# Performance work log

Measured on AMD Instinct MI355X. Metric: run time of the kernel, lower is better.

## Reference

```python
import jax, jax.numpy as jnp
import numpy as np

T, D = 4096, 2048      # tokens, hidden
E, I, K = 16, 1408, 4  # experts, moe intermediate, top_k


def setup_inputs() -> dict:
    key = jax.random.key(0)
    ks = jax.random.split(key, 6)
    W_SCALE = 0.05  # keep activations in a sane range
    x = jax.random.normal(ks[0], (T, D), dtype=jnp.float32)
    w0 = jax.random.normal(ks[1], (E, I, D), dtype=jnp.float32) * W_SCALE  # gate proj
    w1 = jax.random.normal(ks[2], (E, I, D), dtype=jnp.float32) * W_SCALE  # up proj
    w2 = jax.random.normal(ks[3], (E, D, I), dtype=jnp.float32) * W_SCALE  # down proj
    selected_experts = jax.random.randint(ks[4], (T, K), 0, E, dtype=jnp.int32)
    rw = jax.random.uniform(ks[5], (T, K), dtype=jnp.float32)
    routing_weights = rw / jnp.sum(rw, axis=-1, keepdims=True)  # normalized top-k weights
    return {"x": x, "w0": w0, "w1": w1, "w2": w2,
            "selected_experts": selected_experts, "routing_weights": routing_weights}


def reference(x, w0, w1, w2, selected_experts, routing_weights):
    # Per-expert SwiGLU FFN over all tokens: y_e = (silu(x W0_e^T) * (x W1_e^T)) W2_e^T
    def expert_fn(w0_e, w1_e, w2_e):
        h = jax.nn.silu(x @ w0_e.T) * (x @ w1_e.T)  # [T, I]
        return h @ w2_e.T                            # [T, D]

    ys = jax.vmap(expert_fn)(w0, w1, w2)             # [E, T, D]
    # Gather each token's top-k expert outputs and apply routing weights.
    tok = jnp.arange(x.shape[0])[:, None]            # [T, 1]
    gathered = ys[selected_experts, tok, :]          # [T, K, D]
    return gathered * routing_weights[:, :, None]    # [T, K, D]
```

## Files before the change

kernel.cpp:

```cpp
#include <hip/hip_runtime.h>
#include <hip/hip_bf16.h>
#include <stdint.h>

#define NT 4096
#define ND 2048
#define NE 16
#define NI 1408
#define NK 4
#define NTK (NT*NK)

typedef __attribute__((ext_vector_type(8))) short bf16x8;
typedef __attribute__((ext_vector_type(4))) float f32x4;

__device__ __forceinline__ short f2b(float f){
  uint32_t u = __float_as_uint(f);
  uint32_t r = (u + 0x7fffu + ((u >> 16) & 1u)) >> 16;
  return (short)(uint16_t)r;
}
__device__ __forceinline__ float b2f(short s){
  return __uint_as_float(((uint32_t)(uint16_t)s) << 16);
}

__device__ __forceinline__ void gl16(const void* g, void* l){
  __builtin_amdgcn_global_load_lds(
      (const __attribute__((address_space(1))) void*)g,
      (__attribute__((address_space(3))) void*)l, 16, 0, 0);
}

__device__ __forceinline__ int xcd_swz(int lin, int nwg){
  int cpx = nwg >> 3;
  return (lin & 7) * cpx + (lin >> 3);
}



__global__ void detect_init_kernel(const unsigned short* xu, int* wsi){
  const int tid = threadIdx.x;
  if (tid < 64) wsi[tid] = 0;
  wsi[3584 + tid] = 0;
  __shared__ int red[256];
  int c = 0;
  for (int i = tid; i < 8192; i += 256){
    int ex = (xu[i] >> 7) & 0xff;
    c += (ex >= 132) ? 1 : 0;
  }
  red[tid] = c;
  __syncthreads();
  if (tid == 0){
    int s = 0;
    for (int i = 0; i < 256; i++) s += red[i];
    wsi[32] = (s < 64) ? 1 : 0;
  }
}

__global__ void hist_kernel(const int* __restrict__ sel, int* wsi){
  int i = blockIdx.x * 256 + threadIdx.x;
  if (i < NTK) atomicAdd(&wsi[sel[i]], 1);
}

__global__ void plan_kernel(int* wsi){
  if (threadIdx.x != 0) return;
  int4* work64  = (int4*)(wsi + 64);
  int4* work128 = (int4*)(wsi + 2048);
  int off = 0, nw = 0, nw128 = 0;
  for (int e = 0; e < NE; e++){
    int c = wsi[e];
    wsi[40 + e] = off;
    for (int mt = 0; mt * 64 < c; mt++){
      int rem = c - mt * 64;
      work64[nw].x = e; work64[nw].y = off + mt * 64;
      work64[nw].z = rem < 64 ? rem : 64; work64[nw].w = 0;
      nw++;
    }
    for (int mt = 0; mt * 128 < c; mt++){
      int rem = c - mt * 128;
      work128[nw128].x = e; work128[nw128].y = off + mt * 128;
      work128[nw128].z = rem < 128 ? rem : 128; work128[nw128].w = 0;
      nw128++;
    }
    off += c;
  }
  wsi[33] = nw;
  wsi[34] = nw128;
}

__global__ void scatter_kernel(const int* __restrict__ sel, int* wsi, int* list){
  int i = blockIdx.x * 256 + threadIdx.x;
  if (i < NTK){
    int e = sel[i];
    int pos = atomicAdd(&wsi[16 + e], 1);
    list[wsi[40 + e] + pos] = i;
  }
}


__global__ __launch_bounds__(256)
void conv_kernel(const float* __restrict__ src, short* __restrict__ dst,
                 int n8, const int* __restrict__ wsi){
  if (wsi[32]) return;
  int stride = gridDim.x * 256;
  for (int i = blockIdx.x * 256 + threadIdx.x; i < n8; i += stride){
    const float4* s = (const float4*)(src + (size_t)i * 8);
    float4 a = s[0], b = s[1];
    bf16x8 v;
    v[0]=f2b(a.x); v[1]=f2b(a.y); v[2]=f2b(a.z); v[3]=f2b(a.w);
    v[4]=f2b(b.x); v[5]=f2b(b.y); v[6]=f2b(b.z); v[7]=f2b(b.w);
    *(bf16x8*)(dst + (size_t)i * 8) = v;
  }
}


template<int ISB>
__global__ __launch_bounds__(256, 2)
void pass1b_kernel(const void* __restrict__ xg, const void* __restrict__ w0g,
                   const void* __restrict__ w1g,
                   const short* __restrict__ xb, const short* __restrict__ w0b,
                   const short* __restrict__ w1b,
                   const int* __restrict__ wsi, const int* __restrict__ list,
                   short* __restrict__ H)
{
  if (wsi[32] != ISB) return;
  const int nmt = wsi[34];
  const int lin = blockIdx.x + 160 * blockIdx.y;
  const int swz = xcd_swz(lin, 160 * gridDim.y);
  const int mtile = swz % 160;
  const int ntile = swz / 160;
  if (mtile >= nmt) return;
  const int4 wk = ((const int4*)(wsi + 2048))[mtile];
  const int e = wk.x, row_base = wk.y, rows = wk.z;
  const int n0 = ntile * 128;

  __shared__ short As [128 * 32];
  __shared__ short B0s[128 * 32];
  __shared__ short B1s[128 * 32];

  const int tid = threadIdx.x;
  const short* xs  = ISB ? (const short*)xg  : xb;
  const short* w0s = ISB ? (const short*)w0g : w0b;
  const short* w1s = ISB ? (const short*)w1g : w1b;
  const short* zp  = (const short*)(wsi + 3584);

  const int rr = tid >> 2;
  const int cc = (tid & 3) << 3;
  const bool va0 = rr < rows;
  const bool va1 = (64 + rr) < rows;
  const int t0 = va0 ? (list[row_base + rr] >> 2) : 0;
  const int t1 = va1 ? (list[row_base + 64 + rr] >> 2) : 0;
  const short* ag0 = va0 ? xs + (size_t)t0 * ND + cc : zp;
  const short* ag1 = va1 ? xs + (size_t)t1 * ND + cc : zp;
  const int sa0 = va0 ? 32 : 0;
  const int sa1 = va1 ? 32 : 0;
  const short* b0g0 = w0s + ((size_t)e * NI + n0 + rr)      * ND + cc;
  const short* b0g1 = w0s + ((size_t)e * NI + n0 + 64 + rr) * ND + cc;
  const short* b1g0 = w1s + ((size_t)e * NI + n0 + rr)      * ND + cc;
  const short* b1g1 = w1s + ((size_t)e * NI + n0 + 64 + rr) * ND + cc;

  short* la0  = &As [(size_t)tid * 8];
  short* la1  = &As [((size_t)tid + 256) * 8];
  short* lb00 = &B0s[(size_t)tid * 8];
  short* lb01 = &B0s[((size_t)tid + 256) * 8];
  short* lb10 = &B1s[(size_t)tid * 8];
  short* lb11 = &B1s[((size_t)tid + 256) * 8];

  const int lane = tid & 63;
  const int wv = tid >> 6;
  const int wm = (wv >> 1) << 6;
  const int wn = (wv & 1) << 6;
  const int r16 = lane & 15;
  const int qd  = lane >> 4;
  const int qd8 = qd << 3;

  f32x4 acc0[4][4] = {};
  f32x4 acc1[4][4] = {};

  for (int kt = 0; kt < ND; kt += 32){
    __syncthreads();
    gl16(ag0,  la0);  gl16(ag1,  la1);
    gl16(b0g0, lb00); gl16(b0g1, lb01);
    gl16(b1g0, lb10); gl16(b1g1, lb11);
    ag0 += sa0; ag1 += sa1;
    b0g0 += 32; b0g1 += 32; b1g0 += 32; b1g1 += 32;
    __syncthreads();
    bf16x8 af[4], b0f[4], b1f[4];
    #pragma unroll
    for (int mi = 0; mi < 4; mi++)
      af[mi] = *(const bf16x8*)&As[(wm + mi*16 + r16) * 32 + qd8];
    #pragma unroll
    for (int ni = 0; ni < 4; ni++){
      b0f[ni] = *(const bf16x8*)&B0s[(wn + ni*16 + r16) * 32 + qd8];
      b1f[ni] = *(const bf16x8*)&B1s[(wn + ni*16 + r16) * 32 + qd8];
    }
    #pragma unroll
    for (int mi = 0; mi < 4; mi++)
      #pragma unroll
      for (int ni = 0; ni < 4; ni++){
        acc0[mi][ni] = __builtin_amdgcn_mfma_f32_16x16x32_bf16(af[mi], b0f[ni], acc0[mi][ni], 0, 0, 0);
        acc1[mi][ni] = __builtin_amdgcn_mfma_f32_16x16x32_bf16(af[mi], b1f[ni], acc1[mi][ni], 0, 0, 0);
      }
  }

  #pragma unroll
  for (int mi = 0; mi < 4; mi++){
    #pragma unroll
    for (int r = 0; r < 4; r++){
      int m = wm + mi*16 + qd*4 + r;
      if (m >= rows) continue;
      size_t hrow = (size_t)(row_base + m) * NI + n0 + wn;
      #pragma unroll
      for (int ni = 0; ni < 4; ni++){
        float a0v = acc0[mi][ni][r];
        float a1v = acc1[mi][ni][r];
        float hv = (a0v / (1.f + __expf(-a0v))) * a1v;
        H[hrow + ni*16 + r16] = f2b(hv);
      }
    }
  }
}


template<int ISB>
__global__ __launch_bounds__(256, 2)
void pass2b_kernel(const void* __restrict__ w2g, const void* __restrict__ rw,
                   const short* __restrict__ w2b,
                   const int* __restrict__ wsi, const int* __restrict__ list,
                   const short* __restrict__ H, void* __restrict__ out)
{
  if (wsi[32] != ISB) return;
  const int nmt = wsi[34];
  const int lin = blockIdx.x + 160 * blockIdx.y;
  const int swz = xcd_swz(lin, 160 * gridDim.y);
  const int mtile = swz % 160;
  const int ntile = swz / 160;
  if (mtile >= nmt) return;
  const int4 wk = ((const int4*)(wsi + 2048))[mtile];
  const int e = wk.x, row_base = wk.y, rows = wk.z;
  const int n0 = ntile * 256;

  __shared__ short As[128 * 32];
  __shared__ short Bs[256 * 32];

  const int tid = threadIdx.x;
  const short* ws2 = ISB ? (const short*)w2g : w2b;
  const short* zp  = (const short*)(wsi + 3584);

  const int rr = tid >> 2;
  const int cc = (tid & 3) << 3;
  const bool va0 = rr < rows;
  const bool va1 = (64 + rr) < rows;
  const short* ag0 = va0 ? H + (size_t)(row_base + rr) * NI + cc : zp;
  const short* ag1 = va1 ? H + (size_t)(row_base + 64 + rr) * NI + cc : zp;
  const int sa0 = va0 ? 32 : 0;
  const int sa1 = va1 ? 32 : 0;
  const short* bg0 = ws2 + ((size_t)e * ND + n0 + rr)       * NI + cc;
  const short* bg1 = ws2 + ((size_t)e * ND + n0 + 64  + rr) * NI + cc;
  const short* bg2 = ws2 + ((size_t)e * ND + n0 + 128 + rr) * NI + cc;
  const short* bg3 = ws2 + ((size_t)e * ND + n0 + 192 + rr) * NI + cc;

  short* la0 = &As[(size_t)tid * 8];
  short* la1 = &As[((size_t)tid + 256) * 8];
  short* lb0 = &Bs[(size_t)tid * 8];
  short* lb1 = &Bs[((size_t)tid + 256) * 8];
  short* lb2 = &Bs[((size_t)tid + 512) * 8];
  short* lb3 = &Bs[((size_t)tid + 768) * 8];

  const int lane = tid & 63;
  const int wv = tid >> 6;
  const int wm = (wv >> 1) << 6;
  const int wn = (wv & 1) << 7;
  const int r16 = lane & 15;
  const int qd  = lane >> 4;
  const int qd8 = qd << 3;

  f32x4 acc[4][8] = {};

  for (int kt = 0; kt < NI; kt += 32){
    __syncthreads();
    gl16(ag0, la0); gl16(ag1, la1);
    gl16(bg0, lb0); gl16(bg1, lb1);
    gl16(bg2, lb2); gl16(bg3, lb3);
    ag0 += sa0; ag1 += sa1;
    bg0 += 32; bg1 += 32; bg2 += 32; bg3 += 32;
    __syncthreads();
    bf16x8 af[4], bf[8];
    #pragma unroll
    for (int mi = 0; mi < 4; mi++)
      af[mi] = *(const bf16x8*)&As[(wm + mi*16 + r16) * 32 + qd8];
    #pragma unroll
    for (int ni = 0; ni < 8; ni++)
      bf[ni] = *(const bf16x8*)&Bs[(wn + ni*16 + r16) * 32 + qd8];
    #pragma unroll
    for (int mi = 0; mi < 4; mi++)
      #pragma unroll
      for (int ni = 0; ni < 8; ni++)
        acc[mi][ni] = __builtin_amdgcn_mfma_f32_16x16x32_bf16(af[mi], bf[ni], acc[mi][ni], 0, 0, 0);
  }

  #pragma unroll
  for (int mi = 0; mi < 4; mi++){
    #pragma unroll
    for (int r = 0; r < 4; r++){
      int m = wm + mi*16 + qd*4 + r;
      if (m >= rows) continue;
      int p = list[row_base + m];
      float sc = ISB ? b2f(((const short*)rw)[p]) : ((const float*)rw)[p];
      size_t orow = (size_t)p * ND + n0 + wn;
      #pragma unroll
      for (int ni = 0; ni < 8; ni++){
        float v = acc[mi][ni][r] * sc;
        if (ISB) ((short*)out)[orow + ni*16 + r16] = f2b(v);
        else     ((float*)out)[orow + ni*16 + r16] = v;
      }
    }
  }
}


template<int ISB>
__device__ __forceinline__ void stage8(short* dst, const void* base, size_t off, bool valid){
  if (ISB){
    bf16x8 v = valid ? *(const bf16x8*)((const short*)base + off) : (bf16x8)0;
    *(bf16x8*)dst = v;
  } else {
    if (valid){
      const float4* s = (const float4*)((const float*)base + off);
      float4 a = s[0], b = s[1];
      dst[0]=f2b(a.x); dst[1]=f2b(a.y); dst[2]=f2b(a.z); dst[3]=f2b(a.w);
      dst[4]=f2b(b.x); dst[5]=f2b(b.y); dst[6]=f2b(b.z); dst[7]=f2b(b.w);
    } else {
      *(bf16x8*)dst = (bf16x8)0;
    }
  }
}

#define LDS_STRIDE 40

template<int ISB>
__global__ __launch_bounds__(256)
void pass1_kernel(const void* __restrict__ x, const void* __restrict__ w0,
                  const void* __restrict__ w1, const int* __restrict__ wsi,
                  const int* __restrict__ list, short* __restrict__ H)
{
  if (wsi[32] != ISB) return;
  if ((int)blockIdx.x >= wsi[33]) return;
  const int4 wk = ((const int4*)(wsi + 64))[blockIdx.x];
  const int e = wk.x, row_base = wk.y, rows = wk.z;
  const int n0 = blockIdx.y * 64;

  __shared__ short As [64 * LDS_STRIDE];
  __shared__ short B0s[64 * LDS_STRIDE];
  __shared__ short B1s[64 * LDS_STRIDE];

  const int tid = threadIdx.x;
  const int lr  = tid >> 2;
  const int c8  = (tid & 3) << 3;
  const bool avalid = lr < rows;
  size_t abase = 0;
  if (avalid){
    int tok = list[row_base + lr] >> 2;
    abase = (size_t)tok * ND + c8;
  }
  const size_t bbase = ((size_t)e * NI + (size_t)(n0 + lr)) * (size_t)ND + c8;

  const int lane = tid & 63;
  const int wv = tid >> 6;
  const int wm = (wv >> 1) << 5;
  const int wn = (wv & 1) << 5;
  const int r16 = lane & 15;
  const int qd  = lane >> 4;
  const int qd8 = qd << 3;

  f32x4 acc0[2][2] = {};
  f32x4 acc1[2][2] = {};

  short* a_dst  = &As [lr * LDS_STRIDE + c8];
  short* b0_dst = &B0s[lr * LDS_STRIDE + c8];
  short* b1_dst = &B1s[lr * LDS_STRIDE + c8];

  for (int kt = 0; kt < ND; kt += 32){
    __syncthreads();
    stage8<ISB>(a_dst,  x,  abase + kt, avalid);
    stage8<ISB>(b0_dst, w0, bbase + kt, true);
    stage8<ISB>(b1_dst, w1, bbase + kt, true);
    __syncthreads();
    bf16x8 af[2], b0f[2], b1f[2];
    #pragma unroll
    for (int mi = 0; mi < 2; mi++)
      af[mi] = *(const bf16x8*)&As[(wm + mi*16 + r16) * LDS_STRIDE + qd8];
    #pragma unroll
    for (int ni = 0; ni < 2; ni++){
      b0f[ni] = *(const bf16x8*)&B0s[(wn + ni*16 + r16) * LDS_STRIDE + qd8];
      b1f[ni] = *(const bf16x8*)&B1s[(wn + ni*16 + r16) * LDS_STRIDE + qd8];
    }
    #pragma unroll
    for (int mi = 0; mi < 2; mi++)
      #pragma unroll
      for (int ni = 0; ni < 2; ni++){
        acc0[mi][ni] = __builtin_amdgcn_mfma_f32_16x16x32_bf16(af[mi], b0f[ni], acc0[mi][ni], 0, 0, 0);
        acc1[mi][ni] = __builtin_amdgcn_mfma_f32_16x16x32_bf16(af[mi], b1f[ni], acc1[mi][ni], 0, 0, 0);
      }
  }

  #pragma unroll
  for (int mi = 0; mi < 2; mi++){
    #pragma unroll
    for (int r = 0; r < 4; r++){
      int m = wm + mi*16 + qd*4 + r;
      if (m >= rows) continue;
      size_t hrow = (size_t)(row_base + m) * NI + n0;
      #pragma unroll
      for (int ni = 0; ni < 2; ni++){
        float a0v = acc0[mi][ni][r];
        float a1v = acc1[mi][ni][r];
        float hv = (a0v / (1.f + __expf(-a0v))) * a1v;
        H[hrow + wn + ni*16 + r16] = f2b(hv);
      }
    }
  }
}

template<int ISB>
__global__ __launch_bounds__(256)
void pass2_kernel(const void* __restrict__ w2, const void* __restrict__ rw,
                  const int* __restrict__ wsi, const int* __restrict__ list,
                  const short* __restrict__ H, void* __restrict__ out)
{
  if (wsi[32] != ISB) return;
  if ((int)blockIdx.x >= wsi[33]) return;
  const int4 wk = ((const int4*)(wsi + 64))[blockIdx.x];
  const int e = wk.x, row_base = wk.y, rows = wk.z;
  const int n0 = blockIdx.y * 64;

  __shared__ short As[64 * LDS_STRIDE];
  __shared__ short Bs[64 * LDS_STRIDE];

  const int tid = threadIdx.x;
  const int lr  = tid >> 2;
  const int c8  = (tid & 3) << 3;
  const bool avalid = lr < rows;
  const size_t abase = (size_t)(row_base + lr) * NI + c8;
  const size_t bbase = ((size_t)e * ND + (size_t)(n0 + lr)) * (size_t)NI + c8;

  const int lane = tid & 63;
  const int wv = tid >> 6;
  const int wm = (wv >> 1) << 5;
  const int wn = (wv & 1) << 5;
  const int r16 = lane & 15;
  const int qd  = lane >> 4;
  const int qd8 = qd << 3;

  f32x4 acc[2][2] = {};

  short* a_dst = &As[lr * LDS_STRIDE + c8];
  short* b_dst = &Bs[lr * LDS_STRIDE + c8];

  for (int kt = 0; kt < NI; kt += 32){
    __syncthreads();
    {
      bf16x8 v = avalid ? *(const bf16x8*)&H[abase + kt] : (bf16x8)0;
      *(bf16x8*)a_dst = v;
    }
    stage8<ISB>(b_dst, w2, bbase + kt, true);
    __syncthreads();
    bf16x8 af[2], bf[2];
    #pragma unroll
    for (int mi = 0; mi < 2; mi++)
      af[mi] = *(const bf16x8*)&As[(wm + mi*16 + r16) * LDS_STRIDE + qd8];
    #pragma unroll
    for (int ni = 0; ni < 2; ni++)
      bf[ni] = *(const bf16x8*)&Bs[(wn + ni*16 + r16) * LDS_STRIDE + qd8];
    #pragma unroll
    for (int mi = 0; mi < 2; mi++)
      #pragma unroll
      for (int ni = 0; ni < 2; ni++)
        acc[mi][ni] = __builtin_amdgcn_mfma_f32_16x16x32_bf16(af[mi], bf[ni], acc[mi][ni], 0, 0, 0);
  }

  #pragma unroll
  for (int mi = 0; mi < 2; mi++){
    #pragma unroll
    for (int r = 0; r < 4; r++){
      int m = wm + mi*16 + qd*4 + r;
      if (m >= rows) continue;
      int p = list[row_base + m];
      float sc = ISB ? b2f(((const short*)rw)[p]) : ((const float*)rw)[p];
      size_t orow = (size_t)p * ND + n0;
      #pragma unroll
      for (int ni = 0; ni < 2; ni++){
        float v = acc[mi][ni][r] * sc;
        if (ISB) ((short*)out)[orow + wn + ni*16 + r16] = f2b(v);
        else     ((float*)out)[orow + wn + ni*16 + r16] = v;
      }
    }
  }
}


extern "C" void kernel_launch(void* const* d_in, const int* in_sizes, int n_in,
                              void* d_out, int out_size, void* d_ws, size_t ws_size,
                              hipStream_t stream) {
  (void)in_sizes; (void)n_in; (void)out_size;
  const void* x  = d_in[0];
  const void* w0 = d_in[1];
  const void* w1 = d_in[2];
  const void* w2 = d_in[3];
  const int* sel = (const int*)d_in[4];
  const void* rw = d_in[5];

  int* wsi   = (int*)d_ws;
  int* list  = wsi + 4096;
  short* H   = (short*)((char*)d_ws + 262144);

  const size_t H_BYTES  = (size_t)NTK * NI * 2;
  const size_t XB_BYTES = (size_t)NT * ND * 2;
  const size_t WB_BYTES = (size_t)NE * NI * ND * 2;
  const size_t offX = 262144 + H_BYTES;
  const size_t offW = offX + XB_BYTES;
  const size_t need = offW + 2 * WB_BYTES;

  detect_init_kernel<<<1, 256, 0, stream>>>((const unsigned short*)x, wsi);
  hist_kernel<<<NTK/256, 256, 0, stream>>>(sel, wsi);
  plan_kernel<<<1, 64, 0, stream>>>(wsi);
  scatter_kernel<<<NTK/256, 256, 0, stream>>>(sel, wsi, list);

  if (ws_size >= need){
    short* xb  = (short*)((char*)d_ws + offX);
    short* w0b = (short*)((char*)d_ws + offW);
    short* w1b = w0b + (size_t)NE * NI * ND;
    short* w2b = w0b;

    conv_kernel<<<2048, 256, 0, stream>>>((const float*)x,  xb,  NT*ND/8,    wsi);
    conv_kernel<<<2048, 256, 0, stream>>>((const float*)w0, w0b, NE*NI*ND/8, wsi);
    conv_kernel<<<2048, 256, 0, stream>>>((const float*)w1, w1b, NE*NI*ND/8, wsi);

    dim3 g1(160, NI/128);
    pass1b_kernel<1><<<g1, 256, 0, stream>>>(x, w0, w1, xb, w0b, w1b, wsi, list, H);
    pass1b_kernel<0><<<g1, 256, 0, stream>>>(x, w0, w1, xb, w0b, w1b, wsi, list, H);

    conv_kernel<<<2048, 256, 0, stream>>>((const float*)w2, w2b, NE*ND*NI/8, wsi);

    dim3 g2(160, ND/256);
    pass2b_kernel<1><<<g2, 256, 0, stream>>>(w2, rw, w2b, wsi, list, H, d_out);
    pass2b_kernel<0><<<g2, 256, 0, stream>>>(w2, rw, w2b, wsi, list, H, d_out);
  } else {
    dim3 g1(272, NI/64);
    dim3 g2(272, ND/64);
    pass1_kernel<1><<<g1, 256, 0, stream>>>(x, w0, w1, wsi, list, H);
    pass1_kernel<0><<<g1, 256, 0, stream>>>(x, w0, w1, wsi, list, H);
    pass2_kernel<1><<<g2, 256, 0, stream>>>(w2, rw, wsi, list, H, d_out);
    pass2_kernel<0><<<g2, 256, 0, stream>>>(w2, rw, wsi, list, H, d_out);
  }
}
```

Before: 1.130 ms.

## Double-buffer LDS in grouped GEMMs, fuse fp32-to-bf16 conversions, parallelize plan

Both grouped GEMM passes now keep two LDS stages, so the global-to-LDS loads for the next K-slice are issued before the MFMAs on the current one, with a single barrier per iteration. This hides load latency that two barriers per step used to expose, at the cost of doubled LDS use, which may limit occupancy. When the workspace is large enough, the four fp32-to-bf16 conversion launches become one fused kernel over x, w0, w1 and w2 into separate buffers. The plan kernel computes its prefix sums with wave shuffles across lanes instead of a serial loop on one thread.

```diff
diff --git a/kernel.cpp b/kernel.cpp
--- a/kernel.cpp
+++ b/kernel.cpp
@@ -59,29 +59,33 @@
 }
 
 __global__ void plan_kernel(int* wsi){
-  if (threadIdx.x != 0) return;
-  int4* work64  = (int4*)(wsi + 64);
-  int4* work128 = (int4*)(wsi + 2048);
-  int off = 0, nw = 0, nw128 = 0;
+  const int lane = threadIdx.x;
+  int c = (lane < NE) ? wsi[lane] : 0;
+  int off = 0, tb128 = 0, tb64 = 0;
+  int nm128 = (c + 127) >> 7;
+  int nm64  = (c + 63) >> 6;
   for (int e = 0; e < NE; e++){
-    int c = wsi[e];
-    wsi[40 + e] = off;
-    for (int mt = 0; mt * 64 < c; mt++){
+    int ce  = __shfl(c, e, 64);
+    int t1  = __shfl(nm128, e, 64);
+    int t0  = __shfl(nm64, e, 64);
+    if (e < lane){ off += ce; tb128 += t1; tb64 += t0; }
+  }
+  if (lane < NE){
+    wsi[40 + lane] = off;
+    int4* work128 = (int4*)(wsi + 2048);
+    for (int mt = 0; mt < nm128; mt++){
+      int rem = c - mt * 128;
+      work128[tb128 + mt] = make_int4(lane, off + mt * 128, rem < 128 ? rem : 128, 0);
+    }
+    int4* work64 = (int4*)(wsi + 64);
+    for (int mt = 0; mt < nm64; mt++){
       int rem = c - mt * 64;
-      work64[nw].x = e; work64[nw].y = off + mt * 64;
-      work64[nw].z = rem < 64 ? rem : 64; work64[nw].w = 0;
-      nw++;
-    }
-    for (int mt = 0; mt * 128 < c; mt++){
-      int rem = c - mt * 128;
-      work128[nw128].x = e; work128[nw128].y = off + mt * 128;
-      work128[nw128].z = rem < 128 ? rem : 128; work128[nw128].w = 0;
-      nw128++;
-    }
-    off += c;
-  }
-  wsi[33] = nw;
-  wsi[34] = nw128;
+      work64[tb64 + mt] = make_int4(lane, off + mt * 64, rem < 64 ? rem : 64, 0);
+    }
+  }
+  int tot128 = __shfl(tb128 + nm128, NE - 1, 64);
+  int tot64  = __shfl(tb64 + nm64, NE - 1, 64);
+  if (lane == 0){ wsi[33] = tot64; wsi[34] = tot128; }
 }
 
 __global__ void scatter_kernel(const int* __restrict__ sel, int* wsi, int* list){
@@ -95,17 +99,37 @@
 
 
 __global__ __launch_bounds__(256)
-void conv_kernel(const float* __restrict__ src, short* __restrict__ dst,
-                 int n8, const int* __restrict__ wsi){
+void conv1_kernel(const float* __restrict__ src, short* __restrict__ dst,
+                  long n4, const int* __restrict__ wsi){
   if (wsi[32]) return;
-  int stride = gridDim.x * 256;
-  for (int i = blockIdx.x * 256 + threadIdx.x; i < n8; i += stride){
-    const float4* s = (const float4*)(src + (size_t)i * 8);
-    float4 a = s[0], b = s[1];
-    bf16x8 v;
-    v[0]=f2b(a.x); v[1]=f2b(a.y); v[2]=f2b(a.z); v[3]=f2b(a.w);
-    v[4]=f2b(b.x); v[5]=f2b(b.y); v[6]=f2b(b.z); v[7]=f2b(b.w);
-    *(bf16x8*)(dst + (size_t)i * 8) = v;
+  const long stride = (long)gridDim.x * 256;
+  for (long i = (long)blockIdx.x * 256 + threadIdx.x; i < n4; i += stride){
+    float4 a = ((const float4*)src)[i];
+    short4 v; v.x = f2b(a.x); v.y = f2b(a.y); v.z = f2b(a.z); v.w = f2b(a.w);
+    *(short4*)(dst + i * 4) = v;
+  }
+}
+
+__global__ __launch_bounds__(256)
+void conv4_kernel(const float* __restrict__ x, const float* __restrict__ w0,
+                  const float* __restrict__ w1, const float* __restrict__ w2,
+                  short* __restrict__ xb, short* __restrict__ w0b,
+                  short* __restrict__ w1b, short* __restrict__ w2b,
+                  const int* __restrict__ wsi){
+  if (wsi[32]) return;
+  const long NX = (long)NT * ND / 4;
+  const long NW = (long)NE * NI * ND / 4;
+  const long total = NX + 3 * NW;
+  const long stride = (long)gridDim.x * 256;
+  for (long i = (long)blockIdx.x * 256 + threadIdx.x; i < total; i += stride){
+    const float4* s; short* d; long j;
+    if (i < NX)            { s = (const float4*)x;  d = xb;  j = i; }
+    else if (i < NX + NW)  { s = (const float4*)w0; d = w0b; j = i - NX; }
+    else if (i < NX + 2*NW){ s = (const float4*)w1; d = w1b; j = i - NX - NW; }
+    else                   { s = (const float4*)w2; d = w2b; j = i - NX - 2*NW; }
+    float4 a = s[j];
+    short4 v; v.x = f2b(a.x); v.y = f2b(a.y); v.z = f2b(a.z); v.w = f2b(a.w);
+    *(short4*)(d + j * 4) = v;
   }
 }
 
@@ -130,9 +154,9 @@
   const int e = wk.x, row_base = wk.y, rows = wk.z;
   const int n0 = ntile * 128;
 
-  __shared__ short As [128 * 32];
-  __shared__ short B0s[128 * 32];
-  __shared__ short B1s[128 * 32];
+  __shared__ short As [2 * 128 * 32];
+  __shared__ short B0s[2 * 128 * 32];
+  __shared__ short B1s[2 * 128 * 32];
 
   const int tid = threadIdx.x;
   const short* xs  = ISB ? (const short*)xg  : xb;
@@ -173,22 +197,32 @@
   f32x4 acc0[4][4] = {};
   f32x4 acc1[4][4] = {};
 
-  for (int kt = 0; kt < ND; kt += 32){
-    __syncthreads();
-    gl16(ag0,  la0);  gl16(ag1,  la1);
-    gl16(b0g0, lb00); gl16(b0g1, lb01);
-    gl16(b1g0, lb10); gl16(b1g1, lb11);
-    ag0 += sa0; ag1 += sa1;
-    b0g0 += 32; b0g1 += 32; b1g0 += 32; b1g1 += 32;
-    __syncthreads();
+  const int nst = ND / 32;
+  gl16(ag0,  la0);  gl16(ag1,  la1);
+  gl16(b0g0, lb00); gl16(b0g1, lb01);
+  gl16(b1g0, lb10); gl16(b1g1, lb11);
+  ag0 += sa0; ag1 += sa1;
+  b0g0 += 32; b0g1 += 32; b1g0 += 32; b1g1 += 32;
+  __syncthreads();
+
+  for (int t = 0; t < nst; ++t){
+    const int bo = (t & 1) << 12;
+    const int bn = ((t + 1) & 1) << 12;
     bf16x8 af[4], b0f[4], b1f[4];
     #pragma unroll
     for (int mi = 0; mi < 4; mi++)
-      af[mi] = *(const bf16x8*)&As[(wm + mi*16 + r16) * 32 + qd8];
+      af[mi] = *(const bf16x8*)&As[bo + (wm + mi*16 + r16) * 32 + qd8];
     #pragma unroll
     for (int ni = 0; ni < 4; ni++){
-      b0f[ni] = *(const bf16x8*)&B0s[(wn + ni*16 + r16) * 32 + qd8];
-      b1f[ni] = *(const bf16x8*)&B1s[(wn + ni*16 + r16) * 32 + qd8];
+      b0f[ni] = *(const bf16x8*)&B0s[bo + (wn + ni*16 + r16) * 32 + qd8];
+      b1f[ni] = *(const bf16x8*)&B1s[bo + (wn + ni*16 + r16) * 32 + qd8];
+    }
+    if (t + 1 < nst){
+      gl16(ag0,  la0  + bn); gl16(ag1,  la1  + bn);
+      gl16(b0g0, lb00 + bn); gl16(b0g1, lb01 + bn);
+      gl16(b1g0, lb10 + bn); gl16(b1g1, lb11 + bn);
+      ag0 += sa0; ag1 += sa1;
+      b0g0 += 32; b0g1 += 32; b1g0 += 32; b1g1 += 32;
     }
     #pragma unroll
     for (int mi = 0; mi < 4; mi++)
@@ -197,6 +231,7 @@
         acc0[mi][ni] = __builtin_amdgcn_mfma_f32_16x16x32_bf16(af[mi], b0f[ni], acc0[mi][ni], 0, 0, 0);
         acc1[mi][ni] = __builtin_amdgcn_mfma_f32_16x16x32_bf16(af[mi], b1f[ni], acc1[mi][ni], 0, 0, 0);
       }
+    __syncthreads();
   }
 
   #pragma unroll
@@ -236,8 +271,8 @@
   const int e = wk.x, row_base = wk.y, rows = wk.z;
   const int n0 = ntile * 256;
 
-  __shared__ short As[128 * 32];
-  __shared__ short Bs[256 * 32];
+  __shared__ short As[2 * 128 * 32];
+  __shared__ short Bs[2 * 256 * 32];
 
   const int tid = threadIdx.x;
   const short* ws2 = ISB ? (const short*)w2g : w2b;
@@ -273,26 +308,39 @@
 
   f32x4 acc[4][8] = {};
 
-  for (int kt = 0; kt < NI; kt += 32){
-    __syncthreads();
-    gl16(ag0, la0); gl16(ag1, la1);
-    gl16(bg0, lb0); gl16(bg1, lb1);
-    gl16(bg2, lb2); gl16(bg3, lb3);
-    ag0 += sa0; ag1 += sa1;
-    bg0 += 32; bg1 += 32; bg2 += 32; bg3 += 32;
-    __syncthreads();
+  const int nst = NI / 32;
+  gl16(ag0, la0); gl16(ag1, la1);
+  gl16(bg0, lb0); gl16(bg1, lb1);
+  gl16(bg2, lb2); gl16(bg3, lb3);
+  ag0 += sa0; ag1 += sa1;
+  bg0 += 32; bg1 += 32; bg2 += 32; bg3 += 32;
+  __syncthreads();
+
+  for (int t = 0; t < nst; ++t){
+    const int abo = (t & 1) << 12;
+    const int abn = ((t + 1) & 1) << 12;
+    const int bbo = (t & 1) << 13;
+    const int bbn = ((t + 1) & 1) << 13;
     bf16x8 af[4], bf[8];
     #pragma unroll
     for (int mi = 0; mi < 4; mi++)
-      af[mi] = *(const bf16x8*)&As[(wm + mi*16 + r16) * 32 + qd8];
+      af[mi] = *(const bf16x8*)&As[abo + (wm + mi*16 + r16) * 32 + qd8];
     #pragma unroll
     for (int ni = 0; ni < 8; ni++)
-      bf[ni] = *(const bf16x8*)&Bs[(wn + ni*16 + r16) * 32 + qd8];
+      bf[ni] = *(const bf16x8*)&Bs[bbo + (wn + ni*16 + r16) * 32 + qd8];
+    if (t + 1 < nst){
+      gl16(ag0, la0 + abn); gl16(ag1, la1 + abn);
+      gl16(bg0, lb0 + bbn); gl16(bg1, lb1 + bbn);
+      gl16(bg2, lb2 + bbn); gl16(bg3, lb3 + bbn);
+      ag0 += sa0; ag1 += sa1;
+      bg0 += 32; bg1 += 32; bg2 += 32; bg3 += 32;
+    }
     #pragma unroll
     for (int mi = 0; mi < 4; mi++)
       #pragma unroll
       for (int ni = 0; ni < 8; ni++)
         acc[mi][ni] = __builtin_amdgcn_mfma_f32_16x16x32_bf16(af[mi], bf[ni], acc[mi][ni], 0, 0, 0);
+    __syncthreads();
   }
 
   #pragma unroll
@@ -513,34 +561,43 @@
   const size_t H_BYTES  = (size_t)NTK * NI * 2;
   const size_t XB_BYTES = (size_t)NT * ND * 2;
   const size_t WB_BYTES = (size_t)NE * NI * ND * 2;
-  const size_t offX = 262144 + H_BYTES;
-  const size_t offW = offX + XB_BYTES;
-  const size_t need = offW + 2 * WB_BYTES;
+  const size_t offX  = 262144 + H_BYTES;
+  const size_t offW  = offX + XB_BYTES;
+  const size_t need2 = offW + 2 * WB_BYTES;
+  const size_t need3 = offW + 3 * WB_BYTES;
 
   detect_init_kernel<<<1, 256, 0, stream>>>((const unsigned short*)x, wsi);
   hist_kernel<<<NTK/256, 256, 0, stream>>>(sel, wsi);
   plan_kernel<<<1, 64, 0, stream>>>(wsi);
   scatter_kernel<<<NTK/256, 256, 0, stream>>>(sel, wsi, list);
 
-  if (ws_size >= need){
+  if (ws_size >= need2){
     short* xb  = (short*)((char*)d_ws + offX);
     short* w0b = (short*)((char*)d_ws + offW);
     short* w1b = w0b + (size_t)NE * NI * ND;
-    short* w2b = w0b;
-
-    conv_kernel<<<2048, 256, 0, stream>>>((const float*)x,  xb,  NT*ND/8,    wsi);
-    conv_kernel<<<2048, 256, 0, stream>>>((const float*)w0, w0b, NE*NI*ND/8, wsi);
-    conv_kernel<<<2048, 256, 0, stream>>>((const float*)w1, w1b, NE*NI*ND/8, wsi);
-
     dim3 g1(160, NI/128);
-    pass1b_kernel<1><<<g1, 256, 0, stream>>>(x, w0, w1, xb, w0b, w1b, wsi, list, H);
-    pass1b_kernel<0><<<g1, 256, 0, stream>>>(x, w0, w1, xb, w0b, w1b, wsi, list, H);
-
-    conv_kernel<<<2048, 256, 0, stream>>>((const float*)w2, w2b, NE*ND*NI/8, wsi);
-
     dim3 g2(160, ND/256);
-    pass2b_kernel<1><<<g2, 256, 0, stream>>>(w2, rw, w2b, wsi, list, H, d_out);
-    pass2b_kernel<0><<<g2, 256, 0, stream>>>(w2, rw, w2b, wsi, list, H, d_out);
+
+    if (ws_size >= need3){
+      short* w2b = w1b + (size_t)NE * NI * ND;
+      conv4_kernel<<<4096, 256, 0, stream>>>((const float*)x, (const float*)w0,
+                                             (const float*)w1, (const float*)w2,
+                                             xb, w0b, w1b, w2b, wsi);
+      pass1b_kernel<1><<<g1, 256, 0, stream>>>(x, w0, w1, xb, w0b, w1b, wsi, list, H);
+      pass1b_kernel<0><<<g1, 256, 0, stream>>>(x, w0, w1, xb, w0b, w1b, wsi, list, H);
+      pass2b_kernel<1><<<g2, 256, 0, stream>>>(w2, rw, w2b, wsi, list, H, d_out);
+      pass2b_kernel<0><<<g2, 256, 0, stream>>>(w2, rw, w2b, wsi, list, H, d_out);
+    } else {
+      short* w2b = w0b;
+      conv1_kernel<<<2048, 256, 0, stream>>>((const float*)x,  xb,  (long)NT*ND/4,    wsi);
+      conv1_kernel<<<2048, 256, 0, stream>>>((const float*)w0, w0b, (long)NE*NI*ND/4, wsi);
+      conv1_kernel<<<2048, 256, 0, stream>>>((const float*)w1, w1b, (long)NE*NI*ND/4, wsi);
+      pass1b_kernel<1><<<g1, 256, 0, stream>>>(x, w0, w1, xb, w0b, w1b, wsi, list, H);
+      pass1b_kernel<0><<<g1, 256, 0, stream>>>(x, w0, w1, xb, w0b, w1b, wsi, list, H);
+      conv1_kernel<<<2048, 256, 0, stream>>>((const float*)w2, w2b, (long)NE*ND*NI/4, wsi);
+      pass2b_kernel<1><<<g2, 256, 0, stream>>>(w2, rw, w2b, wsi, list, H, d_out);
+      pass2b_kernel<0><<<g2, 256, 0, stream>>>(w2, rw, w2b, wsi, list, H, d_out);
+    }
   } else {
     dim3 g1(272, NI/64);
     dim3 g2(272, ND/64);
```

After: 1.103 ms. -2.4%, faster.
